# Kernel optimization log

Hardware: AMD Instinct MI355X
Metric: run time of the kernel (lower is better)

Reference implementation:

```python
import jax, jax.numpy as jnp
import numpy as np

B, K, C, O, I = 32, 1024, 64, 32, 32  # batch, num_capsules, num_classes, out_dim, in_dim
NUM_ROUTING = 3


def squash(x, axis=-1):
    sq = jnp.sum(x * x, axis=axis, keepdims=True)
    return (sq / (1.0 + sq)) * x / jnp.sqrt(sq + 1e-8)


def setup_inputs() -> dict:
    key = jax.random.key(0)
    kx, kw = jax.random.split(key)
    x = jax.random.normal(kx, (B, K, I), dtype=jnp.float32)
    W = jax.random.normal(kw, (K, C, O, I), dtype=jnp.float32) * 0.01
    return {"x": x, "W": W}


def reference(x, W):
    # u_hat[b,k,c,o] = sum_i W[k,c,o,i] * x[b,k,i]  (the torch repeat+matmul)
    u_hat = jnp.einsum('kcoi,bki->bkco', W, x)  # [B,K,C,O]
    b_ij = jnp.zeros((B, K, C, 1), dtype=x.dtype)
    c_ij = None
    v_j = None
    for i in range(NUM_ROUTING):
        c_ij = jax.nn.softmax(b_ij, axis=2)              # softmax over classes
        s_j = jnp.sum(c_ij * u_hat, axis=1, keepdims=True)  # [B,1,C,O]
        v_j = squash(s_j, axis=-1)
        if i < NUM_ROUTING - 1:
            agreement = jnp.sum(u_hat * v_j, axis=-1, keepdims=True)  # [B,K,C,1]
            b_ij = b_ij + agreement
    return v_j[:, 0], c_ij[..., 0]  # ([B,C,O], [B,K,C])
```

## Files before the change

### kernel.cpp

```cpp
#include <hip/hip_runtime.h>
#include <stdint.h>

#define Bb 32
#define Kk 1024
#define Cc 64
#define Oo 32
#define Ii 32

typedef __attribute__((ext_vector_type(8))) short bf16x8;
typedef __attribute__((ext_vector_type(4))) float f32x4;

__device__ __forceinline__ short f2bf(float f) {
    uint32_t u = __builtin_bit_cast(uint32_t, f);
    u += 0x7fffu + ((u >> 16) & 1u);
    return (short)(u >> 16);
}
__device__ __forceinline__ float bflo(uint32_t u) { return __builtin_bit_cast(float, u << 16); }
__device__ __forceinline__ float bfhi(uint32_t u) { return __builtin_bit_cast(float, u & 0xffff0000u); }
__device__ __forceinline__ uint32_t pk2(float a, float b) {
    return (uint32_t)(uint16_t)f2bf(a) | ((uint32_t)(uint16_t)f2bf(b) << 16);
}


__global__ __launch_bounds__(256) void k_xT(const float* __restrict__ x,
                                            uint32_t* __restrict__ xT) {
    const int k = blockIdx.x;
    const int tid = threadIdx.x;
    const int b = tid >> 3;
    const int i8 = (tid & 7) * 4;
    const float* xp = x + ((size_t)b * Kk + k) * Ii + i8;
    f32x4 v = *(const f32x4*)xp;
    uint32_t* dst = xT + (size_t)k * 512 + b * 16 + i8 / 2;
    dst[0] = pk2(v.x, v.y);
    dst[1] = pk2(v.z, v.w);
}

__global__ __launch_bounds__(256) void k_uhat(const uint32_t* __restrict__ xT,
                                              const float* __restrict__ W,
                                              uint32_t* __restrict__ uh,
                                              float* __restrict__ part0) {
    const int kchunk = blockIdx.x & 63;
    const int cgroup = blockIdx.x >> 6;
    const int lane = threadIdx.x & 63;
    const int wave = threadIdx.x >> 6;
    const int c = cgroup * 4 + wave;
    const int m = lane & 15;
    const int q = lane >> 4;

    float acc[16];
#pragma unroll
    for (int i = 0; i < 16; ++i) acc[i] = 0.f;

    for (int kl = 0; kl < 16; ++kl) {
        const int k = kchunk * 16 + kl;
        const uint32_t* xp = xT + (size_t)k * 512 + m * 16 + q * 4;
        bf16x8 b0 = *(const bf16x8*)xp;
        bf16x8 b1 = *(const bf16x8*)(xp + 256);
        bf16x8 a0, a1;
        {
            const float* wp = W + (size_t)((k * Cc + c) * Oo + m) * Ii + q * 8;
            f32x4 u0 = __builtin_nontemporal_load((const f32x4*)wp);
            f32x4 u1 = __builtin_nontemporal_load((const f32x4*)(wp + 4));
            f32x4 u2 = __builtin_nontemporal_load((const f32x4*)(wp + 512));
            f32x4 u3 = __builtin_nontemporal_load((const f32x4*)(wp + 516));
            bf16x8 t;
            t[0] = f2bf(u0.x); t[1] = f2bf(u0.y); t[2] = f2bf(u0.z); t[3] = f2bf(u0.w);
            t[4] = f2bf(u1.x); t[5] = f2bf(u1.y); t[6] = f2bf(u1.z); t[7] = f2bf(u1.w);
            a0 = t;
            t[0] = f2bf(u2.x); t[1] = f2bf(u2.y); t[2] = f2bf(u2.z); t[3] = f2bf(u2.w);
            t[4] = f2bf(u3.x); t[5] = f2bf(u3.y); t[6] = f2bf(u3.z); t[7] = f2bf(u3.w);
            a1 = t;
        }
        const f32x4 z = {0.f, 0.f, 0.f, 0.f};
        f32x4 d0 = __builtin_amdgcn_mfma_f32_16x16x32_bf16(a0, b0, z, 0, 0, 0);
        f32x4 d1 = __builtin_amdgcn_mfma_f32_16x16x32_bf16(a0, b1, z, 0, 0, 0);
        f32x4 d2 = __builtin_amdgcn_mfma_f32_16x16x32_bf16(a1, b0, z, 0, 0, 0);
        f32x4 d3 = __builtin_amdgcn_mfma_f32_16x16x32_bf16(a1, b1, z, 0, 0, 0);

        uint4 p0, p1;
        p0.x = pk2(d0.x, d0.y); p0.y = pk2(d0.z, d0.w);
        p0.z = pk2(d1.x, d1.y); p0.w = pk2(d1.z, d1.w);
        p1.x = pk2(d2.x, d2.y); p1.y = pk2(d2.z, d2.w);
        p1.z = pk2(d3.x, d3.y); p1.w = pk2(d3.z, d3.w);
        uint32_t* dst = uh + (size_t)(k * Cc + c) * 512 + lane * 4;
        *(uint4*)dst = p0;
        *(uint4*)(dst + 256) = p1;

        acc[0]  += d0.x; acc[1]  += d0.y; acc[2]  += d0.z; acc[3]  += d0.w;
        acc[4]  += d1.x; acc[5]  += d1.y; acc[6]  += d1.z; acc[7]  += d1.w;
        acc[8]  += d2.x; acc[9]  += d2.y; acc[10] += d2.z; acc[11] += d2.w;
        acc[12] += d3.x; acc[13] += d3.y; acc[14] += d3.z; acc[15] += d3.w;
    }
#pragma unroll
    for (int t = 0; t < 4; ++t) {
        f32x4 v = {acc[t * 4 + 0], acc[t * 4 + 1], acc[t * 4 + 2], acc[t * 4 + 3]};
        *(f32x4*)&part0[(((size_t)(kchunk * Cc + c)) * 64 + lane) * 16 + t * 4] = v;
    }
}

__global__ __launch_bounds__(256) void k_redA(const float* __restrict__ part0,
                                              float* __restrict__ vfrag) {
    __shared__ float red[4 * 64 * 17];
    const int c = blockIdx.x;
    const int tid = threadIdx.x;
    const int lane = tid & 63;
    const int grp = tid >> 6;

    float acc[16];
#pragma unroll
    for (int i = 0; i < 16; ++i) acc[i] = 0.f;
    for (int ch = grp * 16; ch < grp * 16 + 16; ++ch) {
        const float* p = part0 + (((size_t)(ch * Cc + c)) * 64 + lane) * 16;
#pragma unroll
        for (int t = 0; t < 4; ++t) {
            f32x4 v = *(const f32x4*)(p + t * 4);
            acc[t * 4 + 0] += v.x; acc[t * 4 + 1] += v.y;
            acc[t * 4 + 2] += v.z; acc[t * 4 + 3] += v.w;
        }
    }
#pragma unroll
    for (int i = 0; i < 16; ++i) red[(grp * 64 + lane) * 17 + i] = acc[i];
    __syncthreads();

    if (tid < 64) {
        float a[16];
#pragma unroll
        for (int i = 0; i < 16; ++i)
            a[i] = (red[tid * 17 + i] + red[(64 + tid) * 17 + i]
                  + red[(128 + tid) * 17 + i] + red[(192 + tid) * 17 + i]) * (1.f / 64.f);
        float sq0 = 0.f, sq1 = 0.f;
#pragma unroll
        for (int r = 0; r < 4; ++r) {
            sq0 += a[r] * a[r] + a[8 + r] * a[8 + r];
            sq1 += a[4 + r] * a[4 + r] + a[12 + r] * a[12 + r];
        }
        sq0 += __shfl_xor(sq0, 16); sq0 += __shfl_xor(sq0, 32);
        sq1 += __shfl_xor(sq1, 16); sq1 += __shfl_xor(sq1, 32);
        const float c0 = sq0 / ((1.f + sq0) * sqrtf(sq0 + 1e-8f));
        const float c1 = sq1 / ((1.f + sq1) * sqrtf(sq1 + 1e-8f));
#pragma unroll
        for (int r = 0; r < 4; ++r) {
            a[r] *= c0; a[8 + r] *= c0;
            a[4 + r] *= c1; a[12 + r] *= c1;
        }
        float* vp = vfrag + ((size_t)c * 64 + tid) * 16;
#pragma unroll
        for (int t = 0; t < 4; ++t) {
            f32x4 v = {a[t * 4 + 0], a[t * 4 + 1], a[t * 4 + 2], a[t * 4 + 3]};
            *(f32x4*)(vp + t * 4) = v;
        }
    }
}

template <bool FINAL>
__global__ __launch_bounds__(512) void k_iter(const uint32_t* __restrict__ uh,
                                              const float* __restrict__ vfrag,
                                              float* __restrict__ bbuf,
                                              uint32_t* __restrict__ partB,
                                              float* __restrict__ outc) {
    __shared__ float agr[4 * 64 * 32];
    const int tid = threadIdx.x;
    const int lane = tid & 63;
    const int w = tid >> 6;
    const int m = lane & 15;
    const int q = lane >> 4;
    const int k0 = blockIdx.x * 4;

    for (int cc = 0; cc < 8; ++cc) {
        const int c = w * 8 + cc;
        const float* vp = vfrag + ((size_t)c * 64 + lane) * 16;
        f32x4 vv0 = *(const f32x4*)(vp);
        f32x4 vv1 = *(const f32x4*)(vp + 4);
        f32x4 vv2 = *(const f32x4*)(vp + 8);
        f32x4 vv3 = *(const f32x4*)(vp + 12);
#pragma unroll
        for (int kl = 0; kl < 4; ++kl) {
            const uint32_t* up = uh + (size_t)((k0 + kl) * Cc + c) * 512 + lane * 4;
            uint4 q0 = *(const uint4*)up;
            uint4 q1 = *(const uint4*)(up + 256);
            float p0 = bflo(q0.x) * vv0.x + bfhi(q0.x) * vv0.y
                     + bflo(q0.y) * vv0.z + bfhi(q0.y) * vv0.w
                     + bflo(q1.x) * vv2.x + bfhi(q1.x) * vv2.y
                     + bflo(q1.y) * vv2.z + bfhi(q1.y) * vv2.w;
            float p1 = bflo(q0.z) * vv1.x + bfhi(q0.z) * vv1.y
                     + bflo(q0.w) * vv1.z + bfhi(q0.w) * vv1.w
                     + bflo(q1.z) * vv3.x + bfhi(q1.z) * vv3.y
                     + bflo(q1.w) * vv3.z + bfhi(q1.w) * vv3.w;
            p0 += __shfl_xor(p0, 16);
            p0 += __shfl_xor(p0, 32);
            p1 += __shfl_xor(p1, 16);
            p1 += __shfl_xor(p1, 32);
            if (q == 0) {
                agr[(kl * 64 + c) * 32 + m] = p0;
                agr[(kl * 64 + c) * 32 + 16 + m] = p1;
            }
        }
    }
    __syncthreads();

    if (tid < 128) {
        const int kl = tid >> 5;
        const int b = tid & 31;
        const int k = k0 + kl;
        float row[64];
#pragma unroll
        for (int c = 0; c < 64; ++c) row[c] = agr[(kl * 64 + c) * 32 + b];
        if (!FINAL) {
            float* bp = bbuf + (size_t)(k * Bb + b) * Cc;
#pragma unroll
            for (int c = 0; c < 64; ++c) bp[c] = row[c];
        } else {
            const float* bp = bbuf + (size_t)(k * Bb + b) * Cc;
#pragma unroll
            for (int c = 0; c < 64; ++c) row[c] += bp[c];
        }
        float mx = row[0];
#pragma unroll
        for (int c = 1; c < 64; ++c) mx = fmaxf(mx, row[c]);
        float sum = 0.f;
#pragma unroll
        for (int c = 0; c < 64; ++c) { row[c] = __expf(row[c] - mx); sum += row[c]; }
        const float inv = 1.f / sum;
#pragma unroll
        for (int c = 0; c < 64; ++c) row[c] *= inv;
        if (FINAL) {
            float* op = outc + (size_t)(b * Kk + k) * Cc;
#pragma unroll
            for (int c = 0; c < 64; ++c) op[c] = row[c];
        }
#pragma unroll
        for (int c = 0; c < 64; ++c) agr[(kl * 64 + c) * 32 + b] = row[c];
    }
    __syncthreads();

    const int chunk = blockIdx.x;
    for (int cg = 0; cg < 8; ++cg) {
        const int c = w * 8 + cg;
        float acc[16];
#pragma unroll
        for (int i = 0; i < 16; ++i) acc[i] = 0.f;
#pragma unroll
        for (int kl = 0; kl < 4; ++kl) {
            const uint32_t* up = uh + (size_t)((k0 + kl) * Cc + c) * 512 + lane * 4;
            uint4 q0 = *(const uint4*)up;
            uint4 q1 = *(const uint4*)(up + 256);
            const float w0 = agr[(kl * 64 + c) * 32 + m];
            const float w1 = agr[(kl * 64 + c) * 32 + 16 + m];
            acc[0]  += w0 * bflo(q0.x);  acc[1]  += w0 * bfhi(q0.x);
            acc[2]  += w0 * bflo(q0.y);  acc[3]  += w0 * bfhi(q0.y);
            acc[4]  += w1 * bflo(q0.z);  acc[5]  += w1 * bfhi(q0.z);
            acc[6]  += w1 * bflo(q0.w);  acc[7]  += w1 * bfhi(q0.w);
            acc[8]  += w0 * bflo(q1.x);  acc[9]  += w0 * bfhi(q1.x);
            acc[10] += w0 * bflo(q1.y);  acc[11] += w0 * bfhi(q1.y);
            acc[12] += w1 * bflo(q1.z);  acc[13] += w1 * bfhi(q1.z);
            acc[14] += w1 * bflo(q1.w);  acc[15] += w1 * bfhi(q1.w);
        }
        uint4 o0, o1;
        o0.x = pk2(acc[0],  acc[1]);  o0.y = pk2(acc[2],  acc[3]);
        o0.z = pk2(acc[4],  acc[5]);  o0.w = pk2(acc[6],  acc[7]);
        o1.x = pk2(acc[8],  acc[9]);  o1.y = pk2(acc[10], acc[11]);
        o1.z = pk2(acc[12], acc[13]); o1.w = pk2(acc[14], acc[15]);
        uint32_t* dst = partB + ((size_t)(c * 256 + chunk) * 64 + lane) * 8;
        *(uint4*)dst = o0;
        *(uint4*)(dst + 4) = o1;
    }
}

__global__ __launch_bounds__(256) void k_red1(const uint32_t* __restrict__ partB,
                                              float* __restrict__ part2) {
    __shared__ float red[4 * 64 * 17];
    const int cb = blockIdx.x;
    const int c = cb >> 3;
    const int g = cb & 7;
    const int tid = threadIdx.x;
    const int lane = tid & 63;
    const int ww = tid >> 6;

    float acc[16];
#pragma unroll
    for (int i = 0; i < 16; ++i) acc[i] = 0.f;
    for (int ch = g * 32 + ww * 8; ch < g * 32 + ww * 8 + 8; ++ch) {
        const uint32_t* p = partB + ((size_t)(c * 256 + ch) * 64 + lane) * 8;
        uint4 a = *(const uint4*)p;
        uint4 b = *(const uint4*)(p + 4);
        acc[0]  += bflo(a.x);  acc[1]  += bfhi(a.x);
        acc[2]  += bflo(a.y);  acc[3]  += bfhi(a.y);
        acc[4]  += bflo(a.z);  acc[5]  += bfhi(a.z);
        acc[6]  += bflo(a.w);  acc[7]  += bfhi(a.w);
        acc[8]  += bflo(b.x);  acc[9]  += bfhi(b.x);
        acc[10] += bflo(b.y);  acc[11] += bfhi(b.y);
        acc[12] += bflo(b.z);  acc[13] += bfhi(b.z);
        acc[14] += bflo(b.w);  acc[15] += bfhi(b.w);
    }
#pragma unroll
    for (int i = 0; i < 16; ++i) red[(ww * 64 + lane) * 17 + i] = acc[i];
    __syncthreads();

    if (tid < 64) {
        float a[16];
#pragma unroll
        for (int i = 0; i < 16; ++i)
            a[i] = red[tid * 17 + i] + red[(64 + tid) * 17 + i]
                 + red[(128 + tid) * 17 + i] + red[(192 + tid) * 17 + i];
        float* dst = part2 + ((size_t)cb * 64 + tid) * 16;
#pragma unroll
        for (int t = 0; t < 4; ++t) {
            f32x4 v = {a[t * 4 + 0], a[t * 4 + 1], a[t * 4 + 2], a[t * 4 + 3]};
            *(f32x4*)(dst + t * 4) = v;
        }
    }
}

template <bool FINAL>
__global__ __launch_bounds__(64) void k_red2(const float* __restrict__ part2,
                                             float* __restrict__ vfrag,
                                             float* __restrict__ out_v) {
    const int c = blockIdx.x;
    const int lane = threadIdx.x;
    const int m = lane & 15;
    const int q = lane >> 4;

    float a[16];
#pragma unroll
    for (int i = 0; i < 16; ++i) a[i] = 0.f;
    for (int g = 0; g < 8; ++g) {
        const float* p = part2 + ((size_t)(c * 8 + g) * 64 + lane) * 16;
#pragma unroll
        for (int t = 0; t < 4; ++t) {
            f32x4 v = *(const f32x4*)(p + t * 4);
            a[t * 4 + 0] += v.x; a[t * 4 + 1] += v.y;
            a[t * 4 + 2] += v.z; a[t * 4 + 3] += v.w;
        }
    }
    float sq0 = 0.f, sq1 = 0.f;
#pragma unroll
    for (int r = 0; r < 4; ++r) {
        sq0 += a[r] * a[r] + a[8 + r] * a[8 + r];
        sq1 += a[4 + r] * a[4 + r] + a[12 + r] * a[12 + r];
    }
    sq0 += __shfl_xor(sq0, 16); sq0 += __shfl_xor(sq0, 32);
    sq1 += __shfl_xor(sq1, 16); sq1 += __shfl_xor(sq1, 32);
    const float c0 = sq0 / ((1.f + sq0) * sqrtf(sq0 + 1e-8f));
    const float c1 = sq1 / ((1.f + sq1) * sqrtf(sq1 + 1e-8f));
#pragma unroll
    for (int r = 0; r < 4; ++r) {
        a[r] *= c0; a[8 + r] *= c0;
        a[4 + r] *= c1; a[12 + r] *= c1;
    }
    float* vp = vfrag + ((size_t)c * 64 + lane) * 16;
#pragma unroll
    for (int t = 0; t < 4; ++t) {
        f32x4 v = {a[t * 4 + 0], a[t * 4 + 1], a[t * 4 + 2], a[t * 4 + 3]};
        *(f32x4*)(vp + t * 4) = v;
    }
    if (FINAL) {
#pragma unroll
        for (int t = 0; t < 4; ++t)
#pragma unroll
            for (int r = 0; r < 4; ++r) {
                const int b = (t & 1) * 16 + m;
                const int o = (t >> 1) * 16 + q * 4 + r;
                out_v[((size_t)b * Cc + c) * Oo + o] = a[t * 4 + r];
            }
    }
}

extern "C" void kernel_launch(void* const* d_in, const int* in_sizes, int n_in,
                              void* d_out, int out_size, void* d_ws, size_t ws_size,
                              hipStream_t stream) {
    (void)in_sizes; (void)n_in; (void)out_size;
    const float* x = (const float*)d_in[0];
    const float* W = (const float*)d_in[1];
    float* out_v = (float*)d_out;
    float* out_c = out_v + Bb * Cc * Oo;

    char* ws = (char*)d_ws;
    const size_t UH_BYTES = (size_t)Kk * Cc * 512 * 4;
    const size_t XT_BYTES = (size_t)Kk * 512 * 4;
    const size_t P0_BYTES = (size_t)64 * Cc * 64 * 16 * 4;
    const size_t PB_BYTES = (size_t)Cc * 256 * 64 * 8 * 4;
    const size_t P2_BYTES = (size_t)512 * 64 * 16 * 4;
    const size_t BB_BYTES = (size_t)Kk * Bb * Cc * 4;
    const size_t VF_BYTES = (size_t)Cc * 64 * 16 * 4;

    uint32_t* uh = (uint32_t*)ws;                      ws += UH_BYTES;
    uint32_t* xT = (uint32_t*)ws;                      ws += XT_BYTES;
    float* part0  = (float*)ws;                        ws += P0_BYTES;
    uint32_t* partB = (uint32_t*)ws;                   ws += PB_BYTES;
    float* part2  = (float*)ws;                        ws += P2_BYTES;
    float* bbuf   = (float*)ws;                        ws += BB_BYTES;
    float* vfrag  = (float*)ws;                        ws += VF_BYTES;
    const size_t NEED = UH_BYTES + XT_BYTES + P0_BYTES + PB_BYTES + P2_BYTES + BB_BYTES + VF_BYTES;
    if (ws_size < NEED) return;

    k_xT<<<Kk, 256, 0, stream>>>(x, xT);
    k_uhat<<<1024, 256, 0, stream>>>(xT, W, uh, part0);
    k_redA<<<Cc, 256, 0, stream>>>(part0, vfrag);
    k_iter<false><<<256, 512, 0, stream>>>(uh, vfrag, bbuf, partB, nullptr);
    k_red1<<<512, 256, 0, stream>>>(partB, part2);
    k_red2<false><<<Cc, 64, 0, stream>>>(part2, vfrag, nullptr);
    k_iter<true><<<256, 512, 0, stream>>>(uh, vfrag, bbuf, partB, out_c);
    k_red1<<<512, 256, 0, stream>>>(partB, part2);
    k_red2<true><<<Cc, 64, 0, stream>>>(part2, vfrag, out_v);
}
```

Baseline: 515.5 us.

## Stage u_hat slabs in LDS with register prefetch to read once per iteration

The routing-iteration kernel now loads each capsule's 128KB u_hat slab into shared memory once, with a register-staged prefetch of the next capsule, rather than reading it twice from global memory (once for agreement, once for the weighted sum). The loop over capsules becomes the outer loop, with 8x16 accumulators kept in registers across it. The softmax is split across 4 threads per row with shuffle reductions, and the agreement buffer is padded to avoid bank conflicts. The cost is about 136KB of dynamic LDS per block plus heavy register use (128 accumulators plus 16 prefetch vectors), which limits occupancy and adds extra barriers per capsule.

```diff
diff --git a/kernel.cpp b/kernel.cpp
--- a/kernel.cpp
+++ b/kernel.cpp
@@ -152,13 +152,17 @@
     }
 }
 
+#define ITER_LDS_BYTES (64 * 512 * 4 + 64 * 33 * 4)
 template <bool FINAL>
-__global__ __launch_bounds__(512) void k_iter(const uint32_t* __restrict__ uh,
-                                              const float* __restrict__ vfrag,
-                                              float* __restrict__ bbuf,
-                                              uint32_t* __restrict__ partB,
-                                              float* __restrict__ outc) {
-    __shared__ float agr[4 * 64 * 32];
+__global__ __launch_bounds__(512, 2) void k_iter(const uint32_t* __restrict__ uh,
+                                                 const float* __restrict__ vfrag,
+                                                 float* __restrict__ bbuf,
+                                                 uint32_t* __restrict__ partB,
+                                                 float* __restrict__ outc) {
+    extern __shared__ char smem[];
+    uint32_t* uhs = (uint32_t*)smem;
+    float* agr = (float*)(smem + 64 * 512 * 4);
+
     const int tid = threadIdx.x;
     const int lane = tid & 63;
     const int w = tid >> 6;
@@ -166,16 +170,43 @@
     const int q = lane >> 4;
     const int k0 = blockIdx.x * 4;
 
-    for (int cc = 0; cc < 8; ++cc) {
-        const int c = w * 8 + cc;
-        const float* vp = vfrag + ((size_t)c * 64 + lane) * 16;
-        f32x4 vv0 = *(const f32x4*)(vp);
-        f32x4 vv1 = *(const f32x4*)(vp + 4);
-        f32x4 vv2 = *(const f32x4*)(vp + 8);
-        f32x4 vv3 = *(const f32x4*)(vp + 12);
-#pragma unroll
-        for (int kl = 0; kl < 4; ++kl) {
-            const uint32_t* up = uh + (size_t)((k0 + kl) * Cc + c) * 512 + lane * 4;
+    float acc[8][16];
+#pragma unroll
+    for (int cg = 0; cg < 8; ++cg)
+#pragma unroll
+        for (int i = 0; i < 16; ++i) acc[cg][i] = 0.f;
+
+    uint4 buf[16];
+    {
+        const uint4* src = (const uint4*)(uh + (size_t)k0 * Cc * 512) + tid;
+#pragma unroll
+        for (int i = 0; i < 16; ++i) buf[i] = src[i * 512];
+    }
+
+    for (int kl = 0; kl < 4; ++kl) {
+        const int k = k0 + kl;
+        if (kl) __syncthreads();
+        {
+            uint4* dst = (uint4*)uhs + tid;
+#pragma unroll
+            for (int i = 0; i < 16; ++i) dst[i * 512] = buf[i];
+        }
+        __syncthreads();
+        if (kl < 3) {
+            const uint4* src = (const uint4*)(uh + (size_t)(k + 1) * Cc * 512) + tid;
+#pragma unroll
+            for (int i = 0; i < 16; ++i) buf[i] = src[i * 512];
+        }
+
+#pragma unroll
+        for (int cc = 0; cc < 8; ++cc) {
+            const int c = w * 8 + cc;
+            const float* vp = vfrag + ((size_t)c * 64 + lane) * 16;
+            f32x4 vv0 = *(const f32x4*)(vp);
+            f32x4 vv1 = *(const f32x4*)(vp + 4);
+            f32x4 vv2 = *(const f32x4*)(vp + 8);
+            f32x4 vv3 = *(const f32x4*)(vp + 12);
+            const uint32_t* up = uhs + c * 512 + lane * 4;
             uint4 q0 = *(const uint4*)up;
             uint4 q1 = *(const uint4*)(up + 256);
             float p0 = bflo(q0.x) * vv0.x + bfhi(q0.x) * vv0.y
@@ -191,75 +222,79 @@
             p1 += __shfl_xor(p1, 16);
             p1 += __shfl_xor(p1, 32);
             if (q == 0) {
-                agr[(kl * 64 + c) * 32 + m] = p0;
-                agr[(kl * 64 + c) * 32 + 16 + m] = p1;
+                agr[c * 33 + m] = p0;
+                agr[c * 33 + 16 + m] = p1;
             }
         }
-    }
-    __syncthreads();
-
-    if (tid < 128) {
-        const int kl = tid >> 5;
-        const int b = tid & 31;
-        const int k = k0 + kl;
-        float row[64];
-#pragma unroll
-        for (int c = 0; c < 64; ++c) row[c] = agr[(kl * 64 + c) * 32 + b];
-        if (!FINAL) {
-            float* bp = bbuf + (size_t)(k * Bb + b) * Cc;
-#pragma unroll
-            for (int c = 0; c < 64; ++c) bp[c] = row[c];
-        } else {
-            const float* bp = bbuf + (size_t)(k * Bb + b) * Cc;
-#pragma unroll
-            for (int c = 0; c < 64; ++c) row[c] += bp[c];
-        }
-        float mx = row[0];
-#pragma unroll
-        for (int c = 1; c < 64; ++c) mx = fmaxf(mx, row[c]);
-        float sum = 0.f;
-#pragma unroll
-        for (int c = 0; c < 64; ++c) { row[c] = __expf(row[c] - mx); sum += row[c]; }
-        const float inv = 1.f / sum;
-#pragma unroll
-        for (int c = 0; c < 64; ++c) row[c] *= inv;
-        if (FINAL) {
-            float* op = outc + (size_t)(b * Kk + k) * Cc;
-#pragma unroll
-            for (int c = 0; c < 64; ++c) op[c] = row[c];
-        }
-#pragma unroll
-        for (int c = 0; c < 64; ++c) agr[(kl * 64 + c) * 32 + b] = row[c];
-    }
-    __syncthreads();
+        __syncthreads();
+
+        if (tid < 128) {
+            const int sub = tid & 3;
+            const int b = tid >> 2;
+            const int cbase = sub * 16;
+            float r[16];
+#pragma unroll
+            for (int j = 0; j < 16; ++j) r[j] = agr[(cbase + j) * 33 + b];
+            if (!FINAL) {
+                float* bp = bbuf + (size_t)(k * Bb + b) * Cc + cbase;
+#pragma unroll
+                for (int j = 0; j < 16; ++j) bp[j] = r[j];
+            } else {
+                const float* bp = bbuf + (size_t)(k * Bb + b) * Cc + cbase;
+#pragma unroll
+                for (int j = 0; j < 16; ++j) r[j] += bp[j];
+            }
+            float mx = r[0];
+#pragma unroll
+            for (int j = 1; j < 16; ++j) mx = fmaxf(mx, r[j]);
+            mx = fmaxf(mx, __shfl_xor(mx, 1));
+            mx = fmaxf(mx, __shfl_xor(mx, 2));
+            float sum = 0.f;
+#pragma unroll
+            for (int j = 0; j < 16; ++j) { r[j] = __expf(r[j] - mx); sum += r[j]; }
+            sum += __shfl_xor(sum, 1);
+            sum += __shfl_xor(sum, 2);
+            const float inv = 1.f / sum;
+#pragma unroll
+            for (int j = 0; j < 16; ++j) r[j] *= inv;
+            if (FINAL) {
+                float* op = outc + (size_t)(b * Kk + k) * Cc + cbase;
+#pragma unroll
+                for (int j = 0; j < 16; ++j) op[j] = r[j];
+            }
+#pragma unroll
+            for (int j = 0; j < 16; ++j) agr[(cbase + j) * 33 + b] = r[j];
+        }
+        __syncthreads();
+
+#pragma unroll
+        for (int cg = 0; cg < 8; ++cg) {
+            const int c = w * 8 + cg;
+            const uint32_t* up = uhs + c * 512 + lane * 4;
+            uint4 q0 = *(const uint4*)up;
+            uint4 q1 = *(const uint4*)(up + 256);
+            const float w0 = agr[c * 33 + m];
+            const float w1 = agr[c * 33 + 16 + m];
+            acc[cg][0]  += w0 * bflo(q0.x);  acc[cg][1]  += w0 * bfhi(q0.x);
+            acc[cg][2]  += w0 * bflo(q0.y);  acc[cg][3]  += w0 * bfhi(q0.y);
+            acc[cg][4]  += w1 * bflo(q0.z);  acc[cg][5]  += w1 * bfhi(q0.z);
+            acc[cg][6]  += w1 * bflo(q0.w);  acc[cg][7]  += w1 * bfhi(q0.w);
+            acc[cg][8]  += w0 * bflo(q1.x);  acc[cg][9]  += w0 * bfhi(q1.x);
+            acc[cg][10] += w0 * bflo(q1.y);  acc[cg][11] += w0 * bfhi(q1.y);
+            acc[cg][12] += w1 * bflo(q1.z);  acc[cg][13] += w1 * bfhi(q1.z);
+            acc[cg][14] += w1 * bflo(q1.w);  acc[cg][15] += w1 * bfhi(q1.w);
+        }
+    }
 
     const int chunk = blockIdx.x;
+#pragma unroll
     for (int cg = 0; cg < 8; ++cg) {
         const int c = w * 8 + cg;
-        float acc[16];
-#pragma unroll
-        for (int i = 0; i < 16; ++i) acc[i] = 0.f;
-#pragma unroll
-        for (int kl = 0; kl < 4; ++kl) {
-            const uint32_t* up = uh + (size_t)((k0 + kl) * Cc + c) * 512 + lane * 4;
-            uint4 q0 = *(const uint4*)up;
-            uint4 q1 = *(const uint4*)(up + 256);
-            const float w0 = agr[(kl * 64 + c) * 32 + m];
-            const float w1 = agr[(kl * 64 + c) * 32 + 16 + m];
-            acc[0]  += w0 * bflo(q0.x);  acc[1]  += w0 * bfhi(q0.x);
-            acc[2]  += w0 * bflo(q0.y);  acc[3]  += w0 * bfhi(q0.y);
-            acc[4]  += w1 * bflo(q0.z);  acc[5]  += w1 * bfhi(q0.z);
-            acc[6]  += w1 * bflo(q0.w);  acc[7]  += w1 * bfhi(q0.w);
-            acc[8]  += w0 * bflo(q1.x);  acc[9]  += w0 * bfhi(q1.x);
-            acc[10] += w0 * bflo(q1.y);  acc[11] += w0 * bfhi(q1.y);
-            acc[12] += w1 * bflo(q1.z);  acc[13] += w1 * bfhi(q1.z);
-            acc[14] += w1 * bflo(q1.w);  acc[15] += w1 * bfhi(q1.w);
-        }
         uint4 o0, o1;
-        o0.x = pk2(acc[0],  acc[1]);  o0.y = pk2(acc[2],  acc[3]);
-        o0.z = pk2(acc[4],  acc[5]);  o0.w = pk2(acc[6],  acc[7]);
-        o1.x = pk2(acc[8],  acc[9]);  o1.y = pk2(acc[10], acc[11]);
-        o1.z = pk2(acc[12], acc[13]); o1.w = pk2(acc[14], acc[15]);
+        o0.x = pk2(acc[cg][0],  acc[cg][1]);  o0.y = pk2(acc[cg][2],  acc[cg][3]);
+        o0.z = pk2(acc[cg][4],  acc[cg][5]);  o0.w = pk2(acc[cg][6],  acc[cg][7]);
+        o1.x = pk2(acc[cg][8],  acc[cg][9]);  o1.y = pk2(acc[cg][10], acc[cg][11]);
+        o1.z = pk2(acc[cg][12], acc[cg][13]); o1.w = pk2(acc[cg][14], acc[cg][15]);
         uint32_t* dst = partB + ((size_t)(c * 256 + chunk) * 64 + lane) * 8;
         *(uint4*)dst = o0;
         *(uint4*)(dst + 4) = o1;
@@ -393,13 +428,22 @@
     const size_t NEED = UH_BYTES + XT_BYTES + P0_BYTES + PB_BYTES + P2_BYTES + BB_BYTES + VF_BYTES;
     if (ws_size < NEED) return;
 
+    static bool attr_done = false;
+    if (!attr_done) {
+        hipFuncSetAttribute((const void*)&k_iter<false>,
+                            hipFuncAttributeMaxDynamicSharedMemorySize, ITER_LDS_BYTES);
+        hipFuncSetAttribute((const void*)&k_iter<true>,
+                            hipFuncAttributeMaxDynamicSharedMemorySize, ITER_LDS_BYTES);
+        attr_done = true;
+    }
+
     k_xT<<<Kk, 256, 0, stream>>>(x, xT);
     k_uhat<<<1024, 256, 0, stream>>>(xT, W, uh, part0);
     k_redA<<<Cc, 256, 0, stream>>>(part0, vfrag);
-    k_iter<false><<<256, 512, 0, stream>>>(uh, vfrag, bbuf, partB, nullptr);
+    k_iter<false><<<256, 512, ITER_LDS_BYTES, stream>>>(uh, vfrag, bbuf, partB, nullptr);
     k_red1<<<512, 256, 0, stream>>>(partB, part2);
     k_red2<false><<<Cc, 64, 0, stream>>>(part2, vfrag, nullptr);
-    k_iter<true><<<256, 512, 0, stream>>>(uh, vfrag, bbuf, partB, out_c);
+    k_iter<true><<<256, 512, ITER_LDS_BYTES, stream>>>(uh, vfrag, bbuf, partB, out_c);
     k_red1<<<512, 256, 0, stream>>>(partB, part2);
     k_red2<true><<<Cc, 64, 0, stream>>>(part2, vfrag, out_v);
 }
```

Result: slower. 670.1 us (+30.0%).
